# Kernel tuning notes

Hardware: AMD Instinct MI355X
Metric: run time of the kernel (lower is better)

Reference implementation:

```python
import jax, jax.numpy as jnp
import numpy as np

H = 16
D = 64  # head_dim = 1024 // 16
SCALE = D ** -0.5


def setup_inputs() -> dict:
    key = jax.random.key(0)
    ks = jax.random.split(key, 12)
    B, N, C = 2, 2048, 1024
    s = C ** -0.5
    return {
        "hidden_states": jax.random.normal(ks[0], (B, N, C), jnp.float32),
        "pos_embeds": jax.random.normal(ks[1], (B, N, C), jnp.float32),
        "Wq": jax.random.normal(ks[2], (C, C), jnp.float32) * s,
        "bq": jnp.zeros((C,), jnp.float32),
        "Wk": jax.random.normal(ks[3], (C, C), jnp.float32) * s,
        "bk": jnp.zeros((C,), jnp.float32),
        "Wv": jax.random.normal(ks[4], (C, C), jnp.float32) * s,
        "bv": jnp.zeros((C,), jnp.float32),
        "Wpos": jax.random.normal(ks[5], (C, C), jnp.float32) * s,
        "pos_bias_u": jax.random.normal(ks[6], (H, D), jnp.float32) * 0.1,
        "pos_bias_v": jax.random.normal(ks[7], (H, D), jnp.float32) * 0.1,
        "Wo": jax.random.normal(ks[8], (C, C), jnp.float32) * s,
        "bo": jnp.zeros((C,), jnp.float32),
    }


def reference(hidden_states, pos_embeds, Wq, bq, Wk, bk, Wv, bv, Wpos,
              pos_bias_u, pos_bias_v, Wo, bo):
    B, N, C = hidden_states.shape
    # projections (torch Linear: y = x @ W.T + b), split heads -> (B, N, H, D)
    q = (hidden_states @ Wq.T + bq).reshape(B, N, H, D)
    k = (hidden_states @ Wk.T + bk).reshape(B, N, H, D)
    v = (hidden_states @ Wv.T + bv).reshape(B, N, H, D)
    p = (pos_embeds @ Wpos.T).reshape(B, N, H, D)
    # relative-position biased logits: matrix_ac + matrix_bd
    q_u = q + pos_bias_u  # (B,N,H,D) + (H,D)
    q_v = q + pos_bias_v
    ac = jnp.einsum('bnhd,bmhd->bhnm', q_u, k)
    bd = jnp.einsum('bnhd,bmhd->bhnm', q_v, p)
    attn = jax.nn.softmax((ac + bd) * SCALE, axis=-1)  # (B,H,N,N)
    out = jnp.einsum('bhnm,bmhd->bnhd', attn, v).reshape(B, N, C)
    return out @ Wo.T + bo
```

## Files before the change

### kernel.cpp

```cpp
#include <hip/hip_runtime.h>
#include <hip/hip_bf16.h>


typedef short bf16x8 __attribute__((ext_vector_type(8)));
typedef float f32x4 __attribute__((ext_vector_type(4)));

#define BB 2
#define NN 2048
#define CC 1024
#define HH 16
#define DD 64
#define MM (BB * NN)
#define SC2E 0.18033688f

__device__ __forceinline__ unsigned short f2bf(float f) {
    union { float f; unsigned int u; } x; x.f = f;
    unsigned int r = x.u + 0x7FFFu + ((x.u >> 16) & 1u);
    return (unsigned short)(r >> 16);
}

__device__ __forceinline__ float bf2f(unsigned short s) {
    union { unsigned int u; float f; } x; x.u = ((unsigned int)s) << 16;
    return x.f;
}

__device__ __forceinline__ unsigned int pk2(float a, float b) {
    __hip_bfloat162 h = __float22bfloat162_rn(make_float2(a, b));
    unsigned int u; __builtin_memcpy(&u, &h, 4); return u;
}

typedef __attribute__((address_space(1))) const unsigned int* gas1_t;
typedef __attribute__((address_space(3))) unsigned int* las3_t;

__device__ __forceinline__ void gload_lds16(const unsigned short* g, unsigned short* l) {
    __builtin_amdgcn_global_load_lds((gas1_t)g, (las3_t)l, 16, 0, 0);
}

struct CastArgs {
    const float* src[7];
    unsigned short* dst[7];
    int n4[7];
};
__global__ __launch_bounds__(256) void cast_all(CastArgs a) {
    const int seg = blockIdx.y;
    const int i = blockIdx.x * 256 + threadIdx.x;
    if (i >= a.n4[seg]) return;
    float4 v = ((const float4*)a.src[seg])[i];
    uint2 u;
    u.x = pk2(v.x, v.y);
    u.y = pk2(v.z, v.w);
    ((uint2*)a.dst[seg])[i] = u;
}

struct GemmBatch {
    const unsigned short* A[4];
    const unsigned short* B[4];
    unsigned short* out[4];
    const float* bias[4];
};
__global__ __launch_bounds__(256) void gemm_qkvp(GemmBatch g) {
    constexpr int K = CC;
    __shared__ unsigned short Sh[2 * 128 * 32];
    unsigned short* As = Sh;
    unsigned short* Bs = Sh + 128 * 32;
    const int z = blockIdx.z;
    const unsigned short* __restrict__ A = g.A[z];
    const unsigned short* __restrict__ B = g.B[z];
    unsigned short* __restrict__ out = g.out[z];
    const float* __restrict__ bias = g.bias[z];

    const int t = threadIdx.x;
    const int w = t >> 6, lane = t & 63, l15 = lane & 15, quad = lane >> 4;
    const int m0 = blockIdx.x * 128, n0 = blockIdx.y * 128;
    const int wm = (w >> 1) * 64, wn = (w & 1) * 64;

    f32x4 acc[4][4];
#pragma unroll
    for (int i = 0; i < 4; ++i)
#pragma unroll
        for (int j = 0; j < 4; ++j)
#pragma unroll
            for (int r = 0; r < 4; ++r) acc[i][j][r] = 0.f;

    for (int kb = 0; kb < K; kb += 32) {
        __syncthreads();
#pragma unroll
        for (int j = 0; j < 2; ++j) {
            int id = j * 256 + t;
            int row = id >> 2, c4 = (id & 3) * 8;
            gload_lds16(&A[(size_t)(m0 + row) * K + kb + c4], &As[id * 8]);
            gload_lds16(&B[(size_t)(n0 + row) * K + kb + c4], &Bs[id * 8]);
        }
        __syncthreads();
        bf16x8 af[4], bfr[4];
#pragma unroll
        for (int i = 0; i < 4; ++i)
            af[i] = *(const bf16x8*)&As[(wm + i * 16 + l15) * 32 + quad * 8];
#pragma unroll
        for (int j = 0; j < 4; ++j)
            bfr[j] = *(const bf16x8*)&Bs[(wn + j * 16 + l15) * 32 + quad * 8];
#pragma unroll
        for (int i = 0; i < 4; ++i)
#pragma unroll
            for (int j = 0; j < 4; ++j)
                acc[i][j] = __builtin_amdgcn_mfma_f32_16x16x32_bf16(af[i], bfr[j], acc[i][j], 0, 0, 0);
    }

    if (z != 2) {
        const float sc = (z == 0) ? SC2E : 1.f;
#pragma unroll
        for (int i = 0; i < 4; ++i)
#pragma unroll
            for (int j = 0; j < 4; ++j) {
                const int col = n0 + wn + j * 16 + l15;
                const int row_base = m0 + wm + i * 16 + quad * 4;
                const float bc = bias ? bias[col] : 0.f;
#pragma unroll
                for (int r = 0; r < 4; ++r)
                    out[(size_t)(row_base + r) * CC + col] = f2bf((acc[i][j][r] + bc) * sc);
            }
    } else {
        __syncthreads();
        unsigned short* Tr = &Sh[w * 1152];
        const int bI = (m0 + wm) >> 11, nseq0 = (m0 + wm) & 2047;
        const int colL = lane >> 3;
        const int mL = (lane & 7) * 8;
#pragma unroll
        for (int j = 0; j < 4; ++j) {
            const int col = n0 + wn + j * 16 + l15;
            const float bc = bias[col];
#pragma unroll
            for (int i = 0; i < 4; ++i) {
                uint2 pk;
                pk.x = pk2(acc[i][j][0] + bc, acc[i][j][1] + bc);
                pk.y = pk2(acc[i][j][2] + bc, acc[i][j][3] + bc);
                *(uint2*)&Tr[l15 * 72 + i * 16 + quad * 4] = pk;
            }
#pragma unroll
            for (int p = 0; p < 2; ++p) {
                const int cl = p * 8 + colL;
                uint4 vv = *(const uint4*)&Tr[cl * 72 + mL];
                const int gcol = n0 + wn + j * 16 + cl;
                const int hh = gcol >> 6, dd = gcol & 63;
                *(uint4*)&out[((size_t)(bI * 16 + hh) * 64 + dd) * 2048 + nseq0 + mL] = vv;
            }
        }
    }
}

__global__ __launch_bounds__(256) void fuse_kpc(const unsigned short* __restrict__ k,
                                                const unsigned short* __restrict__ pp,
                                                const float* __restrict__ pbu,
                                                const float* __restrict__ pbv,
                                                unsigned short* __restrict__ kp,
                                                float* __restrict__ c) {
    const int gw = (blockIdx.x * 256 + threadIdx.x) >> 6;
    const int lane = threadIdx.x & 63;
    const int row = gw >> 4, h = gw & 15;
    const size_t off = (size_t)row * CC + h * 64 + lane;
    const float kv = bf2f(k[off]), pv = bf2f(pp[off]);
    kp[off] = f2bf(kv + pv);
    float val = pbu[h * 64 + lane] * kv + pbv[h * 64 + lane] * pv;
#pragma unroll
    for (int o = 1; o < 64; o <<= 1) val += __shfl_xor(val, o);
    if (lane == 0) {
        const int b = row >> 11, n = row & 2047;
        c[((size_t)(b * HH + h)) * NN + n] = val * SC2E;
    }
}

#define PST 80
__global__ __launch_bounds__(256) void attn_kernel(const unsigned short* __restrict__ q,
                                                   const unsigned short* __restrict__ kp,
                                                   const unsigned short* __restrict__ vt,
                                                   const float* __restrict__ cb,
                                                   unsigned short* __restrict__ att) {
    __shared__ unsigned short Ks[64 * 64];
    __shared__ unsigned short Vs[64 * 64];
    __shared__ unsigned short Ps[4][32 * PST];

    const int t = threadIdx.x;
    const int w = t >> 6, lane = t & 63, l15 = lane & 15, quad = lane >> 4;
    const int qt = blockIdx.x, h = blockIdx.y, b = blockIdx.z;
    const int sw = (l15 & 7) * 8;

    bf16x8 qf[2][2];
#pragma unroll
    for (int qb = 0; qb < 2; ++qb) {
        const int qrow = qt * 128 + w * 32 + qb * 16 + l15;
        const size_t qoff = ((size_t)(b * NN + qrow) * HH + h) * DD;
#pragma unroll
        for (int c2 = 0; c2 < 2; ++c2)
            qf[qb][c2] = *(const bf16x8*)&q[qoff + c2 * 32 + quad * 8];
    }

    f32x4 oT[4][2];
    float l_lane[2] = {0.f, 0.f};
#pragma unroll
    for (int db = 0; db < 4; ++db)
#pragma unroll
        for (int qb = 0; qb < 2; ++qb)
#pragma unroll
            for (int r = 0; r < 4; ++r) oT[db][qb][r] = 0.f;

    const size_t kbase = (size_t)b * NN * CC + (size_t)h * DD;
    const size_t vbase = (size_t)(b * HH + h) * DD * NN;
    const size_t cbase = (size_t)(b * HH + h) * NN;

    for (int kt = 0; kt < NN / 64; ++kt) {
        f32x4 c4[4];
#pragma unroll
        for (int t4 = 0; t4 < 4; ++t4)
            c4[t4] = *(const f32x4*)&cb[cbase + kt * 64 + t4 * 16 + quad * 4];

        __syncthreads();
#pragma unroll
        for (int j = 0; j < 2; ++j) {
            int id = j * 256 + t, row = id >> 3, c8 = id & 7;
            int gc = (c8 ^ (row & 7)) * 8;
            gload_lds16(&kp[kbase + (size_t)(kt * 64 + row) * CC + gc], &Ks[id * 8]);
            gload_lds16(&vt[vbase + (size_t)row * NN + kt * 64 + gc], &Vs[id * 8]);
        }
        __syncthreads();

        f32x4 s[2][4];
#pragma unroll
        for (int t4 = 0; t4 < 4; ++t4) {
            s[0][t4] = c4[t4];
            s[1][t4] = c4[t4];
        }
#pragma unroll
        for (int t4 = 0; t4 < 4; ++t4) {
            const int row = t4 * 16 + l15;
#pragma unroll
            for (int c2 = 0; c2 < 2; ++c2) {
                bf16x8 kf = *(const bf16x8*)&Ks[row * 64 + ((c2 * 4 + quad) * 8 ^ sw)];
#pragma unroll
                for (int qb = 0; qb < 2; ++qb)
                    s[qb][t4] = __builtin_amdgcn_mfma_f32_16x16x32_bf16(kf, qf[qb][c2], s[qb][t4], 0, 0, 0);
            }
        }

#pragma unroll
        for (int qb = 0; qb < 2; ++qb) {
            float rs = 0.f;
#pragma unroll
            for (int t4 = 0; t4 < 4; ++t4)
#pragma unroll
                for (int r = 0; r < 4; ++r) {
                    float pv = exp2f(s[qb][t4][r]);
                    s[qb][t4][r] = pv;
                    rs += pv;
                }
            l_lane[qb] += rs;
#pragma unroll
            for (int t4 = 0; t4 < 4; ++t4) {
                uint2 pk;
                pk.x = pk2(s[qb][t4][0], s[qb][t4][1]);
                pk.y = pk2(s[qb][t4][2], s[qb][t4][3]);
                *(uint2*)&Ps[w][(qb * 16 + l15) * PST + t4 * 16 + quad * 4] = pk;
            }
        }

#pragma unroll
        for (int c2 = 0; c2 < 2; ++c2) {
            bf16x8 pf[2];
#pragma unroll
            for (int qb = 0; qb < 2; ++qb)
                pf[qb] = *(const bf16x8*)&Ps[w][(qb * 16 + l15) * PST + c2 * 32 + quad * 8];
#pragma unroll
            for (int db = 0; db < 4; ++db) {
                bf16x8 vf = *(const bf16x8*)&Vs[(db * 16 + l15) * 64 + ((c2 * 4 + quad) * 8 ^ sw)];
#pragma unroll
                for (int qb = 0; qb < 2; ++qb)
                    oT[db][qb] = __builtin_amdgcn_mfma_f32_16x16x32_bf16(vf, pf[qb], oT[db][qb], 0, 0, 0);
            }
        }
    }

#pragma unroll
    for (int qb = 0; qb < 2; ++qb) {
        float l = l_lane[qb];
        l += __shfl_xor(l, 16);
        l += __shfl_xor(l, 32);
        const float inv = 1.f / l;
        const int qrow = qt * 128 + w * 32 + qb * 16 + l15;
        const size_t ob = ((size_t)(b * NN + qrow) * HH + h) * DD;
#pragma unroll
        for (int db = 0; db < 4; ++db) {
            uint2 pk;
            pk.x = pk2(oT[db][qb][0] * inv, oT[db][qb][1] * inv);
            pk.y = pk2(oT[db][qb][2] * inv, oT[db][qb][3] * inv);
            *(uint2*)&att[ob + db * 16 + quad * 4] = pk;
        }
    }
}

__global__ __launch_bounds__(256) void gemm_out(const unsigned short* __restrict__ A,
                                                const unsigned short* __restrict__ B,
                                                float* __restrict__ out,
                                                const float* __restrict__ bias) {
    constexpr int K = CC;
    __shared__ unsigned short As[128 * 32];
    __shared__ unsigned short Bs[64 * 32];
    const int t = threadIdx.x;
    const int w = t >> 6, lane = t & 63, l15 = lane & 15, quad = lane >> 4;
    const int m0 = blockIdx.x * 128, n0 = blockIdx.y * 64;
    const int wm = (w >> 1) * 64, wn = (w & 1) * 32;

    f32x4 acc[4][2];
#pragma unroll
    for (int i = 0; i < 4; ++i)
#pragma unroll
        for (int j = 0; j < 2; ++j)
#pragma unroll
            for (int r = 0; r < 4; ++r) acc[i][j][r] = 0.f;

    for (int kb = 0; kb < K; kb += 32) {
        __syncthreads();
#pragma unroll
        for (int j = 0; j < 2; ++j) {
            int id = j * 256 + t;
            int row = id >> 2, c4 = (id & 3) * 8;
            gload_lds16(&A[(size_t)(m0 + row) * K + kb + c4], &As[id * 8]);
        }
        {
            int row = t >> 2, c4 = (t & 3) * 8;
            gload_lds16(&B[(size_t)(n0 + row) * K + kb + c4], &Bs[t * 8]);
        }
        __syncthreads();
        bf16x8 af[4], bfr[2];
#pragma unroll
        for (int i = 0; i < 4; ++i)
            af[i] = *(const bf16x8*)&As[(wm + i * 16 + l15) * 32 + quad * 8];
#pragma unroll
        for (int j = 0; j < 2; ++j)
            bfr[j] = *(const bf16x8*)&Bs[(wn + j * 16 + l15) * 32 + quad * 8];
#pragma unroll
        for (int i = 0; i < 4; ++i)
#pragma unroll
            for (int j = 0; j < 2; ++j)
                acc[i][j] = __builtin_amdgcn_mfma_f32_16x16x32_bf16(af[i], bfr[j], acc[i][j], 0, 0, 0);
    }

#pragma unroll
    for (int i = 0; i < 4; ++i)
#pragma unroll
        for (int j = 0; j < 2; ++j) {
            const int col = n0 + wn + j * 16 + l15;
            const int row_base = m0 + wm + i * 16 + quad * 4;
            const float bc = bias[col];
#pragma unroll
            for (int r = 0; r < 4; ++r)
                out[(size_t)(row_base + r) * CC + col] = acc[i][j][r] + bc;
        }
}

extern "C" void kernel_launch(void* const* d_in, const int* in_sizes, int n_in,
                              void* d_out, int out_size, void* d_ws, size_t ws_size,
                              hipStream_t stream) {
    const float* hs   = (const float*)d_in[0];
    const float* pos  = (const float*)d_in[1];
    const float* Wq   = (const float*)d_in[2];
    const float* bq   = (const float*)d_in[3];
    const float* Wk   = (const float*)d_in[4];
    const float* bk   = (const float*)d_in[5];
    const float* Wv   = (const float*)d_in[6];
    const float* bv   = (const float*)d_in[7];
    const float* Wpos = (const float*)d_in[8];
    const float* pbu  = (const float*)d_in[9];
    const float* pbv  = (const float*)d_in[10];
    const float* Wo   = (const float*)d_in[11];
    const float* bo   = (const float*)d_in[12];
    float* out = (float*)d_out;

    const size_t nHS = (size_t)MM * CC;
    const size_t nW  = (size_t)CC * CC;

    unsigned short* p = (unsigned short*)d_ws;
    unsigned short* hsb  = p;            p += nHS;
    unsigned short* posb = p;            p += nHS;
    unsigned short* wqb  = p;            p += nW;
    unsigned short* wkb  = p;            p += nW;
    unsigned short* wvb  = p;            p += nW;
    unsigned short* wpb  = p;            p += nW;
    unsigned short* wob  = p;            p += nW;
    unsigned short* qsb  = p;            p += nHS;
    unsigned short* kbf  = p;            p += nHS;
    unsigned short* pbf  = p;            p += nHS;
    unsigned short* kpb  = p;            p += nHS;
    unsigned short* vtb  = p;            p += nHS;
    float* cb = (float*)p;               p += (size_t)BB * HH * NN * 2;
    unsigned short* attb = hsb;

    CastArgs ca;
    ca.src[0] = hs;   ca.dst[0] = hsb;  ca.n4[0] = (int)(nHS / 4);
    ca.src[1] = pos;  ca.dst[1] = posb; ca.n4[1] = (int)(nHS / 4);
    ca.src[2] = Wq;   ca.dst[2] = wqb;  ca.n4[2] = (int)(nW / 4);
    ca.src[3] = Wk;   ca.dst[3] = wkb;  ca.n4[3] = (int)(nW / 4);
    ca.src[4] = Wv;   ca.dst[4] = wvb;  ca.n4[4] = (int)(nW / 4);
    ca.src[5] = Wpos; ca.dst[5] = wpb;  ca.n4[5] = (int)(nW / 4);
    ca.src[6] = Wo;   ca.dst[6] = wob;  ca.n4[6] = (int)(nW / 4);
    dim3 cgrid((unsigned)(nHS / 4 / 256), 7);
    cast_all<<<cgrid, 256, 0, stream>>>(ca);

    GemmBatch gb;
    gb.A[0] = hsb;  gb.B[0] = wqb; gb.out[0] = qsb; gb.bias[0] = bq;
    gb.A[1] = hsb;  gb.B[1] = wkb; gb.out[1] = kbf; gb.bias[1] = bk;
    gb.A[2] = hsb;  gb.B[2] = wvb; gb.out[2] = vtb; gb.bias[2] = bv;
    gb.A[3] = posb; gb.B[3] = wpb; gb.out[3] = pbf; gb.bias[3] = nullptr;
    dim3 ggrid(MM / 128, CC / 128, 4);
    gemm_qkvp<<<ggrid, 256, 0, stream>>>(gb);

    fuse_kpc<<<MM * HH / 4, 256, 0, stream>>>(kbf, pbf, pbu, pbv, kpb, cb);

    dim3 agrid(NN / 128, HH, BB);
    attn_kernel<<<agrid, 256, 0, stream>>>(qsb, kpb, vtb, cb, attb);

    dim3 ogrid(MM / 128, CC / 64);
    gemm_out<<<ogrid, 256, 0, stream>>>(attb, wob, out, bo);
}
```

Measured before the change: 267.0 us.

## Double-buffer K/V tiles and use 512-thread blocks with one query tile per wave

The attention kernel now prefetches the next K/V tile into a second LDS buffer while computing on the current one, which cuts the per-iteration barriers from two to one. Blocks grow to 8 waves, each handling 16 query rows instead of 32. The P staging buffer switches from padding to an XOR swizzle to avoid bank conflicts. Latency hiding should improve, but each wave now reuses its K/V fragment LDS reads across fewer MFMAs, and LDS use per block rises.

```diff
diff --git a/kernel.cpp b/kernel.cpp
--- a/kernel.cpp
+++ b/kernel.cpp
@@ -169,130 +169,111 @@
     }
 }
 
-#define PST 80
-__global__ __launch_bounds__(256) void attn_kernel(const unsigned short* __restrict__ q,
+__global__ __launch_bounds__(512) void attn_kernel(const unsigned short* __restrict__ q,
                                                    const unsigned short* __restrict__ kp,
                                                    const unsigned short* __restrict__ vt,
                                                    const float* __restrict__ cb,
                                                    unsigned short* __restrict__ att) {
-    __shared__ unsigned short Ks[64 * 64];
-    __shared__ unsigned short Vs[64 * 64];
-    __shared__ unsigned short Ps[4][32 * PST];
+    __shared__ unsigned short Ks[2][64 * 64];
+    __shared__ unsigned short Vs[2][64 * 64];
+    __shared__ unsigned short Ps[8][16 * 64];
 
     const int t = threadIdx.x;
     const int w = t >> 6, lane = t & 63, l15 = lane & 15, quad = lane >> 4;
     const int qt = blockIdx.x, h = blockIdx.y, b = blockIdx.z;
     const int sw = (l15 & 7) * 8;
 
-    bf16x8 qf[2][2];
-#pragma unroll
-    for (int qb = 0; qb < 2; ++qb) {
-        const int qrow = qt * 128 + w * 32 + qb * 16 + l15;
+    bf16x8 qf[2];
+    {
+        const int qrow = qt * 128 + w * 16 + l15;
         const size_t qoff = ((size_t)(b * NN + qrow) * HH + h) * DD;
 #pragma unroll
         for (int c2 = 0; c2 < 2; ++c2)
-            qf[qb][c2] = *(const bf16x8*)&q[qoff + c2 * 32 + quad * 8];
-    }
-
-    f32x4 oT[4][2];
-    float l_lane[2] = {0.f, 0.f};
+            qf[c2] = *(const bf16x8*)&q[qoff + c2 * 32 + quad * 8];
+    }
+
+    f32x4 oT[4];
+    float l_lane = 0.f;
 #pragma unroll
     for (int db = 0; db < 4; ++db)
 #pragma unroll
-        for (int qb = 0; qb < 2; ++qb)
-#pragma unroll
-            for (int r = 0; r < 4; ++r) oT[db][qb][r] = 0.f;
+        for (int r = 0; r < 4; ++r) oT[db][r] = 0.f;
 
     const size_t kbase = (size_t)b * NN * CC + (size_t)h * DD;
     const size_t vbase = (size_t)(b * HH + h) * DD * NN;
     const size_t cbase = (size_t)(b * HH + h) * NN;
 
+    const int srow = t >> 3, sc8 = t & 7;
+    const int sgc = (sc8 ^ (srow & 7)) * 8;
+
+    gload_lds16(&kp[kbase + (size_t)srow * CC + sgc], &Ks[0][t * 8]);
+    gload_lds16(&vt[vbase + (size_t)srow * NN + sgc], &Vs[0][t * 8]);
+
     for (int kt = 0; kt < NN / 64; ++kt) {
-        f32x4 c4[4];
+        const int cur = kt & 1;
+        __syncthreads();
+        if (kt + 1 < NN / 64) {
+            gload_lds16(&kp[kbase + (size_t)((kt + 1) * 64 + srow) * CC + sgc], &Ks[cur ^ 1][t * 8]);
+            gload_lds16(&vt[vbase + (size_t)srow * NN + (kt + 1) * 64 + sgc], &Vs[cur ^ 1][t * 8]);
+        }
+
+        f32x4 s[4];
 #pragma unroll
         for (int t4 = 0; t4 < 4; ++t4)
-            c4[t4] = *(const f32x4*)&cb[cbase + kt * 64 + t4 * 16 + quad * 4];
-
-        __syncthreads();
-#pragma unroll
-        for (int j = 0; j < 2; ++j) {
-            int id = j * 256 + t, row = id >> 3, c8 = id & 7;
-            int gc = (c8 ^ (row & 7)) * 8;
-            gload_lds16(&kp[kbase + (size_t)(kt * 64 + row) * CC + gc], &Ks[id * 8]);
-            gload_lds16(&vt[vbase + (size_t)row * NN + kt * 64 + gc], &Vs[id * 8]);
-        }
-        __syncthreads();
-
-        f32x4 s[2][4];
-#pragma unroll
-        for (int t4 = 0; t4 < 4; ++t4) {
-            s[0][t4] = c4[t4];
-            s[1][t4] = c4[t4];
-        }
+            s[t4] = *(const f32x4*)&cb[cbase + kt * 64 + t4 * 16 + quad * 4];
+
 #pragma unroll
         for (int t4 = 0; t4 < 4; ++t4) {
             const int row = t4 * 16 + l15;
 #pragma unroll
             for (int c2 = 0; c2 < 2; ++c2) {
-                bf16x8 kf = *(const bf16x8*)&Ks[row * 64 + ((c2 * 4 + quad) * 8 ^ sw)];
-#pragma unroll
-                for (int qb = 0; qb < 2; ++qb)
-                    s[qb][t4] = __builtin_amdgcn_mfma_f32_16x16x32_bf16(kf, qf[qb][c2], s[qb][t4], 0, 0, 0);
-            }
-        }
-
-#pragma unroll
-        for (int qb = 0; qb < 2; ++qb) {
-            float rs = 0.f;
-#pragma unroll
-            for (int t4 = 0; t4 < 4; ++t4)
-#pragma unroll
-                for (int r = 0; r < 4; ++r) {
-                    float pv = exp2f(s[qb][t4][r]);
-                    s[qb][t4][r] = pv;
-                    rs += pv;
-                }
-            l_lane[qb] += rs;
-#pragma unroll
-            for (int t4 = 0; t4 < 4; ++t4) {
-                uint2 pk;
-                pk.x = pk2(s[qb][t4][0], s[qb][t4][1]);
-                pk.y = pk2(s[qb][t4][2], s[qb][t4][3]);
-                *(uint2*)&Ps[w][(qb * 16 + l15) * PST + t4 * 16 + quad * 4] = pk;
-            }
+                bf16x8 kf = *(const bf16x8*)&Ks[cur][row * 64 + ((c2 * 4 + quad) * 8 ^ sw)];
+                s[t4] = __builtin_amdgcn_mfma_f32_16x16x32_bf16(kf, qf[c2], s[t4], 0, 0, 0);
+            }
+        }
+
+        float rs = 0.f;
+#pragma unroll
+        for (int t4 = 0; t4 < 4; ++t4)
+#pragma unroll
+            for (int r = 0; r < 4; ++r) {
+                float pv = exp2f(s[t4][r]);
+                s[t4][r] = pv;
+                rs += pv;
+            }
+        l_lane += rs;
+#pragma unroll
+        for (int t4 = 0; t4 < 4; ++t4) {
+            uint2 pk;
+            pk.x = pk2(s[t4][0], s[t4][1]);
+            pk.y = pk2(s[t4][2], s[t4][3]);
+            const int blk = t4 * 2 + (quad >> 1);
+            *(uint2*)&Ps[w][l15 * 64 + ((blk ^ (l15 & 7)) * 8) + (quad & 1) * 4] = pk;
         }
 
 #pragma unroll
         for (int c2 = 0; c2 < 2; ++c2) {
-            bf16x8 pf[2];
-#pragma unroll
-            for (int qb = 0; qb < 2; ++qb)
-                pf[qb] = *(const bf16x8*)&Ps[w][(qb * 16 + l15) * PST + c2 * 32 + quad * 8];
+            bf16x8 pf = *(const bf16x8*)&Ps[w][l15 * 64 + (((c2 * 4 + quad) ^ (l15 & 7)) * 8)];
 #pragma unroll
             for (int db = 0; db < 4; ++db) {
-                bf16x8 vf = *(const bf16x8*)&Vs[(db * 16 + l15) * 64 + ((c2 * 4 + quad) * 8 ^ sw)];
-#pragma unroll
-                for (int qb = 0; qb < 2; ++qb)
-                    oT[db][qb] = __builtin_amdgcn_mfma_f32_16x16x32_bf16(vf, pf[qb], oT[db][qb], 0, 0, 0);
-            }
-        }
-    }
-
-#pragma unroll
-    for (int qb = 0; qb < 2; ++qb) {
-        float l = l_lane[qb];
-        l += __shfl_xor(l, 16);
-        l += __shfl_xor(l, 32);
-        const float inv = 1.f / l;
-        const int qrow = qt * 128 + w * 32 + qb * 16 + l15;
-        const size_t ob = ((size_t)(b * NN + qrow) * HH + h) * DD;
-#pragma unroll
-        for (int db = 0; db < 4; ++db) {
-            uint2 pk;
-            pk.x = pk2(oT[db][qb][0] * inv, oT[db][qb][1] * inv);
-            pk.y = pk2(oT[db][qb][2] * inv, oT[db][qb][3] * inv);
-            *(uint2*)&att[ob + db * 16 + quad * 4] = pk;
-        }
+                bf16x8 vf = *(const bf16x8*)&Vs[cur][(db * 16 + l15) * 64 + ((c2 * 4 + quad) * 8 ^ sw)];
+                oT[db] = __builtin_amdgcn_mfma_f32_16x16x32_bf16(vf, pf, oT[db], 0, 0, 0);
+            }
+        }
+    }
+
+    float l = l_lane;
+    l += __shfl_xor(l, 16);
+    l += __shfl_xor(l, 32);
+    const float inv = 1.f / l;
+    const int qrow = qt * 128 + w * 16 + l15;
+    const size_t ob = ((size_t)(b * NN + qrow) * HH + h) * DD;
+#pragma unroll
+    for (int db = 0; db < 4; ++db) {
+        uint2 pk;
+        pk.x = pk2(oT[db][0] * inv, oT[db][1] * inv);
+        pk.y = pk2(oT[db][2] * inv, oT[db][3] * inv);
+        *(uint2*)&att[ob + db * 16 + quad * 4] = pk;
     }
 }
 
@@ -415,7 +396,7 @@
     fuse_kpc<<<MM * HH / 4, 256, 0, stream>>>(kbf, pbf, pbu, pbv, kpb, cb);
 
     dim3 agrid(NN / 128, HH, BB);
-    attn_kernel<<<agrid, 256, 0, stream>>>(qsb, kpb, vtb, cb, attb);
+    attn_kernel<<<agrid, 512, 0, stream>>>(qsb, kpb, vtb, cb, attb);
 
     dim3 ogrid(MM / 128, CC / 64);
     gemm_out<<<ogrid, 256, 0, stream>>>(attb, wob, out, bo);
```

After: 266.2 us. No clear change (-0.3%).
